# Performance work log

Hardware: AMD Instinct MI355X
Metric: run time of the kernel (lower is better)

Reference implementation:

```python
import jax, jax.numpy as jnp
import numpy as np


def setup_inputs() -> dict:
    key = jax.random.key(0)
    k1, k2 = jax.random.split(key)
    B, D, C = 4096, 128, 64
    score = jax.random.normal(k1, (B, D), dtype=jnp.float32)
    target = jax.random.randint(k2, (B,), 0, C, dtype=jnp.int64)
    alpha = jnp.full((1,), 9.0, dtype=jnp.float32)  # learned margin param
    return {"score": score, "target": target, "alpha": alpha}


def _pairwise_dist(score):
    # squared euclidean: ||xi||^2 + ||xj||^2 - 2 xi.xj, clamped at 0, then sqrt
    mag = jnp.sum(score * score, axis=1)            # [B]
    d2 = mag[:, None] + mag[None, :] - 2.0 * (score @ score.T)
    d2 = jnp.maximum(d2, 0.0)
    # safe sqrt (diagonal is exactly 0; avoid nan grads)
    safe = jnp.where(d2 > 0.0, d2, 1.0)
    return jnp.where(d2 > 0.0, jnp.sqrt(safe), 0.0)  # [B, B]


def reference(score, target, alpha):
    target = target.reshape(-1)
    B = score.shape[0]
    dist = _pairwise_dist(score)                    # [B, B]
    diff = target[:, None] != target[None, :]       # [B, B] negative-pair mask
    # per-anchor sum over negatives of exp(alpha - dist); diagonal excluded (same label)
    nes = jnp.sum(jnp.where(diff, jnp.exp(alpha[0] - dist), 0.0), axis=1)  # [B]
    l_n = jnp.log(nes[:, None] + nes[None, :])      # [B, B]
    # positive pairs i<j with equal labels
    upper = jnp.triu(jnp.ones((B, B), dtype=bool), k=1)
    pos = (~diff) & upper
    terms = jnp.where(pos, jax.nn.relu(l_n + dist) ** 2, 0.0)
    counter = jnp.sum(pos).astype(score.dtype)
    return jnp.sum(terms) / (2.0 * counter)
```

## Files before the change

kernel.cpp:

```cpp
#include <hip/hip_runtime.h>
#include <math.h>

#define BN 4096
#define DD 128
#define NCLS 64
#define PSPLIT 16
#define NPOSB (NCLS * PSPLIT)
#define NJB 32

typedef __attribute__((ext_vector_type(8))) short short8;
typedef __attribute__((ext_vector_type(4))) float f32x4;

__device__ __forceinline__ unsigned short f2bf(float f) {
    unsigned int u = __float_as_uint(f);
    u += 0x7FFFu + ((u >> 16) & 1u);
    return (unsigned short)(u >> 16);
}

__device__ __forceinline__ void gload_lds16(const void* g, void* l) {
    __builtin_amdgcn_global_load_lds(
        (const __attribute__((address_space(1))) unsigned int*)g,
        (__attribute__((address_space(3))) unsigned int*)l, 16, 0, 0);
}


__global__ __launch_bounds__(256)
void prep_kernel(const float* __restrict__ score, unsigned short* __restrict__ sbf,
                 float* __restrict__ mag) {
    int row  = blockIdx.x * 4 + (threadIdx.x >> 6);
    int lane = threadIdx.x & 63;
    float2 v = *reinterpret_cast<const float2*>(score + (size_t)row * DD + lane * 2);
    float s = v.x * v.x + v.y * v.y;
    #pragma unroll
    for (int off = 32; off; off >>= 1) s += __shfl_xor(s, off);
    ushort2 u; u.x = f2bf(v.x); u.y = f2bf(v.y);
    *reinterpret_cast<ushort2*>(sbf + (size_t)row * DD + lane * 2) = u;
    if (lane == 0) mag[row] = s;
}

__global__ __launch_bounds__(256)
void bucket_kernel(const int* __restrict__ target,
                   int* __restrict__ cls_cnt, int* __restrict__ cls_start,
                   int* __restrict__ cls_list) {
    __shared__ int hist[NCLS];
    __shared__ int offs[NCLS];
    int tid = threadIdx.x;
    if (tid < NCLS) hist[tid] = 0;
    __syncthreads();
    for (int i = tid; i < BN; i += 256) atomicAdd(&hist[target[i]], 1);
    __syncthreads();
    if (tid == 0) {
        int run = 0;
        for (int c = 0; c < NCLS; ++c) {
            cls_cnt[c] = hist[c];
            cls_start[c] = run;
            offs[c] = run;
            run += hist[c];
        }
    }
    __syncthreads();
    for (int i = tid; i < BN; i += 256) {
        int p = atomicAdd(&offs[target[i]], 1);
        cls_list[p] = i;
    }
}

__global__ __launch_bounds__(256)
void nes_kernel(const unsigned short* __restrict__ sbf, const int* __restrict__ target,
                const float* __restrict__ alphap, const float* __restrict__ mag,
                float* __restrict__ nes_part) {
    __shared__ __align__(16) unsigned short lds[2 * 128 * 128];
    __shared__ float rowsum[2][128];
    const int tid = threadIdx.x;
    const int w = tid >> 6, lane = tid & 63;
    const int lhi = lane >> 4, llo = lane & 15;
    const int i0 = blockIdx.x * 128, j0 = blockIdx.y * 128;
    const int jb = blockIdx.y;

    #pragma unroll
    for (int t = 0; t < 8; ++t) {
        int rl = w * 32 + t * 4 + lhi;
        int ch = llo ^ (rl & 7);
        const unsigned short* srcA = sbf + (size_t)(i0 + rl) * DD + ch * 8;
        const unsigned short* srcB = sbf + (size_t)(j0 + rl) * DD + ch * 8;
        gload_lds16(srcA, lds + (w * 32 + t * 4) * 128);
        gload_lds16(srcB, lds + 128 * 128 + (w * 32 + t * 4) * 128);
    }
    __syncthreads();

    const int wr = w >> 1, wc = w & 1;
    f32x4 acc[4][4] = {};
    #pragma unroll
    for (int kk = 0; kk < 4; ++kk) {
        short8 a[4], b[4];
        #pragma unroll
        for (int m = 0; m < 4; ++m) {
            int r = wr * 64 + m * 16 + llo;
            int ch = (kk * 4 + lhi) ^ (r & 7);
            a[m] = *reinterpret_cast<const short8*>(lds + r * 128 + ch * 8);
        }
        #pragma unroll
        for (int n = 0; n < 4; ++n) {
            int r = wc * 64 + n * 16 + llo;
            int ch = (kk * 4 + lhi) ^ (r & 7);
            b[n] = *reinterpret_cast<const short8*>(lds + 128 * 128 + r * 128 + ch * 8);
        }
        #pragma unroll
        for (int m = 0; m < 4; ++m)
            #pragma unroll
            for (int n = 0; n < 4; ++n)
                acc[m][n] = __builtin_amdgcn_mfma_f32_16x16x32_bf16(a[m], b[n], acc[m][n], 0, 0, 0);
    }

    const float alpha = alphap[0];
    float mj[4]; int tj[4];
    #pragma unroll
    for (int n = 0; n < 4; ++n) {
        int j = j0 + wc * 64 + n * 16 + llo;
        mj[n] = mag[j]; tj[n] = target[j];
    }
    #pragma unroll
    for (int m = 0; m < 4; ++m) {
        #pragma unroll
        for (int rg = 0; rg < 4; ++rg) {
            int li = wr * 64 + m * 16 + lhi * 4 + rg;
            int i = i0 + li;
            float mi = mag[i];
            int ti = target[i];
            float rs = 0.f;
            #pragma unroll
            for (int n = 0; n < 4; ++n) {
                float d2 = fmaxf(mi + mj[n] - 2.0f * acc[m][n][rg], 0.0f);
                float dist = sqrtf(d2);
                rs += (ti != tj[n]) ? __expf(alpha - dist) : 0.0f;
            }
            rs += __shfl_xor(rs, 1);
            rs += __shfl_xor(rs, 2);
            rs += __shfl_xor(rs, 4);
            rs += __shfl_xor(rs, 8);
            if (llo == 0) rowsum[wc][li] = rs;
        }
    }
    __syncthreads();
    if (tid < 128)
        nes_part[(size_t)jb * BN + i0 + tid] = rowsum[0][tid] + rowsum[1][tid];
}

__global__ __launch_bounds__(256)
void nes_reduce_kernel(const float* __restrict__ nes_part, float* __restrict__ nes) {
    int t = blockIdx.x * 256 + threadIdx.x;
    float s = 0.f;
    #pragma unroll
    for (int k = 0; k < NJB; ++k) s += nes_part[(size_t)k * BN + t];
    nes[t] = s;
}

__global__ __launch_bounds__(256)
void pos_kernel(const float* __restrict__ score, const float* __restrict__ mag,
                const float* __restrict__ nes,
                const int* __restrict__ cls_cnt, const int* __restrict__ cls_start,
                const int* __restrict__ cls_list,
                float* __restrict__ part_sum, unsigned int* __restrict__ part_cnt) {
    __shared__ float ssum[4];
    __shared__ unsigned int scnt[4];
    const int c = blockIdx.x;
    const int n = cls_cnt[c], s0 = cls_start[c];
    const int tid = threadIdx.x;
    const int grp = tid >> 4, llo = tid & 15;
    const int g0 = blockIdx.y * 16 + grp;
    const int nG = 16 * PSPLIT;
    const int nn = n * n;
    float s = 0.f;
    unsigned int cc = 0;
    for (int p = g0; p < nn; p += nG) {
        int a = p / n, b = p - a * n;
        if (b <= a) continue;
        int i = cls_list[s0 + a], j = cls_list[s0 + b];
        const float4* ra = reinterpret_cast<const float4*>(score + (size_t)i * DD) + llo * 2;
        const float4* rb = reinterpret_cast<const float4*>(score + (size_t)j * DD) + llo * 2;
        float4 x0 = ra[0], x1 = ra[1];
        float4 y0 = rb[0], y1 = rb[1];
        float dot = x0.x * y0.x + x0.y * y0.y + x0.z * y0.z + x0.w * y0.w
                  + x1.x * y1.x + x1.y * y1.y + x1.z * y1.z + x1.w * y1.w;
        dot += __shfl_xor(dot, 1);
        dot += __shfl_xor(dot, 2);
        dot += __shfl_xor(dot, 4);
        dot += __shfl_xor(dot, 8);
        if (llo == 0) {
            float d2 = fmaxf(mag[i] + mag[j] - 2.0f * dot, 0.0f);
            float dist = sqrtf(d2);
            float t = __logf(nes[i] + nes[j]) + dist;
            if (t > 0.f) s += t * t;
            cc++;
        }
    }
    #pragma unroll
    for (int off = 1; off < 64; off <<= 1) {
        s += __shfl_xor(s, off);
        cc += __shfl_xor(cc, off);
    }
    if ((tid & 63) == 0) { ssum[tid >> 6] = s; scnt[tid >> 6] = cc; }
    __syncthreads();
    if (tid == 0) {
        int bid = blockIdx.y * NCLS + blockIdx.x;
        part_sum[bid] = ssum[0] + ssum[1] + ssum[2] + ssum[3];
        part_cnt[bid] = scnt[0] + scnt[1] + scnt[2] + scnt[3];
    }
}

__global__ __launch_bounds__(256)
void finalize_kernel(const float* __restrict__ part_sum,
                     const unsigned int* __restrict__ part_cnt,
                     float* __restrict__ out) {
    __shared__ float fs[4];
    __shared__ unsigned int fc[4];
    int tid = threadIdx.x;
    float s = 0.f;
    unsigned int c = 0;
    #pragma unroll
    for (int k = 0; k < NPOSB / 256; ++k) {
        s += part_sum[k * 256 + tid];
        c += part_cnt[k * 256 + tid];
    }
    #pragma unroll
    for (int off = 1; off < 64; off <<= 1) {
        s += __shfl_xor(s, off);
        c += __shfl_xor(c, off);
    }
    if ((tid & 63) == 0) { fs[tid >> 6] = s; fc[tid >> 6] = c; }
    __syncthreads();
    if (tid == 0) {
        float S = fs[0] + fs[1] + fs[2] + fs[3];
        float C = (float)(fc[0] + fc[1] + fc[2] + fc[3]);
        out[0] = S / (2.0f * C);
    }
}

extern "C" void kernel_launch(void* const* d_in, const int* in_sizes, int n_in,
                              void* d_out, int out_size, void* d_ws, size_t ws_size,
                              hipStream_t stream) {
    const float* score  = (const float*)d_in[0];
    const int*   target = (const int*)d_in[1];
    const float* alpha  = (const float*)d_in[2];
    float* out = (float*)d_out;

    unsigned short* sbf = (unsigned short*)d_ws;
    float* mag      = (float*)((char*)d_ws + (size_t)BN * DD * 2);
    float* nes      = mag + BN;
    float* nes_part = nes + BN;
    float* part_sum = nes_part + (size_t)NJB * BN;
    unsigned int* part_cnt = (unsigned int*)(part_sum + NPOSB);
    int* cls_cnt   = (int*)(part_cnt + NPOSB);
    int* cls_start = cls_cnt + NCLS;
    int* cls_list  = cls_start + NCLS;

    prep_kernel<<<BN / 4, 256, 0, stream>>>(score, sbf, mag);
    bucket_kernel<<<1, 256, 0, stream>>>(target, cls_cnt, cls_start, cls_list);
    dim3 g(BN / 128, BN / 128);
    nes_kernel<<<g, 256, 0, stream>>>(sbf, target, alpha, mag, nes_part);
    nes_reduce_kernel<<<BN / 256, 256, 0, stream>>>(nes_part, nes);
    pos_kernel<<<dim3(NCLS, PSPLIT), 256, 0, stream>>>(score, mag, nes,
                                                       cls_cnt, cls_start, cls_list,
                                                       part_sum, part_cnt);
    finalize_kernel<<<1, 256, 0, stream>>>(part_sum, part_cnt, out);
}
```

Measured before the change: 112.6 us.

## Exploit distance symmetry in nes tiles and fuse prep, bucket and reduce kernels

The nes kernel now computes only upper-triangular 128x128 tiles and produces both row and column sums, so the GEMM and exp work is roughly halved. On diagonal tiles it loads the single block once. The partial sums are stored transposed ([row][jb]) and reduced inside pos_kernel, which removes the nes_reduce launch. prep and bucket are merged into one launch, and pos computes d2 directly from the fp32 difference instead of through mag. In exchange, half the grid's blocks exit immediately, and the column-sum shuffles and extra stores add work to each remaining block.

```diff
diff --git a/kernel.cpp b/kernel.cpp
--- a/kernel.cpp
+++ b/kernel.cpp
@@ -25,43 +25,42 @@
 
 
 __global__ __launch_bounds__(256)
-void prep_kernel(const float* __restrict__ score, unsigned short* __restrict__ sbf,
-                 float* __restrict__ mag) {
-    int row  = blockIdx.x * 4 + (threadIdx.x >> 6);
-    int lane = threadIdx.x & 63;
-    float2 v = *reinterpret_cast<const float2*>(score + (size_t)row * DD + lane * 2);
-    float s = v.x * v.x + v.y * v.y;
-    #pragma unroll
-    for (int off = 32; off; off >>= 1) s += __shfl_xor(s, off);
-    ushort2 u; u.x = f2bf(v.x); u.y = f2bf(v.y);
-    *reinterpret_cast<ushort2*>(sbf + (size_t)row * DD + lane * 2) = u;
-    if (lane == 0) mag[row] = s;
-}
-
-__global__ __launch_bounds__(256)
-void bucket_kernel(const int* __restrict__ target,
-                   int* __restrict__ cls_cnt, int* __restrict__ cls_start,
-                   int* __restrict__ cls_list) {
+void prep_bucket_kernel(const float* __restrict__ score, const int* __restrict__ target,
+                        unsigned short* __restrict__ sbf, float* __restrict__ mag,
+                        int* __restrict__ cls_cnt, int* __restrict__ cls_start,
+                        int* __restrict__ cls_list) {
     __shared__ int hist[NCLS];
     __shared__ int offs[NCLS];
-    int tid = threadIdx.x;
-    if (tid < NCLS) hist[tid] = 0;
-    __syncthreads();
-    for (int i = tid; i < BN; i += 256) atomicAdd(&hist[target[i]], 1);
-    __syncthreads();
-    if (tid == 0) {
-        int run = 0;
-        for (int c = 0; c < NCLS; ++c) {
-            cls_cnt[c] = hist[c];
-            cls_start[c] = run;
-            offs[c] = run;
-            run += hist[c];
-        }
-    }
-    __syncthreads();
-    for (int i = tid; i < BN; i += 256) {
-        int p = atomicAdd(&offs[target[i]], 1);
-        cls_list[p] = i;
+    const int tid = threadIdx.x;
+    if (blockIdx.x < BN / 4) {
+        int row  = blockIdx.x * 4 + (tid >> 6);
+        int lane = tid & 63;
+        float2 v = *reinterpret_cast<const float2*>(score + (size_t)row * DD + lane * 2);
+        float s = v.x * v.x + v.y * v.y;
+        #pragma unroll
+        for (int off = 32; off; off >>= 1) s += __shfl_xor(s, off);
+        ushort2 u; u.x = f2bf(v.x); u.y = f2bf(v.y);
+        *reinterpret_cast<ushort2*>(sbf + (size_t)row * DD + lane * 2) = u;
+        if (lane == 0) mag[row] = s;
+    } else {
+        if (tid < NCLS) hist[tid] = 0;
+        __syncthreads();
+        for (int i = tid; i < BN; i += 256) atomicAdd(&hist[target[i]], 1);
+        __syncthreads();
+        if (tid == 0) {
+            int run = 0;
+            for (int c = 0; c < NCLS; ++c) {
+                cls_cnt[c] = hist[c];
+                cls_start[c] = run;
+                offs[c] = run;
+                run += hist[c];
+            }
+        }
+        __syncthreads();
+        for (int i = tid; i < BN; i += 256) {
+            int p = atomicAdd(&offs[target[i]], 1);
+            cls_list[p] = i;
+        }
     }
 }
 
@@ -69,25 +68,29 @@
 void nes_kernel(const unsigned short* __restrict__ sbf, const int* __restrict__ target,
                 const float* __restrict__ alphap, const float* __restrict__ mag,
                 float* __restrict__ nes_part) {
+    const int ib = blockIdx.x, jb = blockIdx.y;
+    if (jb < ib) return;
     __shared__ __align__(16) unsigned short lds[2 * 128 * 128];
     __shared__ float rowsum[2][128];
+    __shared__ float colsum[2][128];
     const int tid = threadIdx.x;
     const int w = tid >> 6, lane = tid & 63;
     const int lhi = lane >> 4, llo = lane & 15;
-    const int i0 = blockIdx.x * 128, j0 = blockIdx.y * 128;
-    const int jb = blockIdx.y;
+    const int i0 = ib * 128, j0 = jb * 128;
+    const bool diag = (ib == jb);
 
     #pragma unroll
     for (int t = 0; t < 8; ++t) {
         int rl = w * 32 + t * 4 + lhi;
         int ch = llo ^ (rl & 7);
-        const unsigned short* srcA = sbf + (size_t)(i0 + rl) * DD + ch * 8;
-        const unsigned short* srcB = sbf + (size_t)(j0 + rl) * DD + ch * 8;
-        gload_lds16(srcA, lds + (w * 32 + t * 4) * 128);
-        gload_lds16(srcB, lds + 128 * 128 + (w * 32 + t * 4) * 128);
-    }
-    __syncthreads();
-
+        gload_lds16(sbf + (size_t)(i0 + rl) * DD + ch * 8, lds + (w * 32 + t * 4) * 128);
+        if (!diag)
+            gload_lds16(sbf + (size_t)(j0 + rl) * DD + ch * 8,
+                        lds + 128 * 128 + (w * 32 + t * 4) * 128);
+    }
+    __syncthreads();
+
+    const unsigned short* bbase = diag ? lds : (lds + 128 * 128);
     const int wr = w >> 1, wc = w & 1;
     f32x4 acc[4][4] = {};
     #pragma unroll
@@ -103,7 +106,7 @@
         for (int n = 0; n < 4; ++n) {
             int r = wc * 64 + n * 16 + llo;
             int ch = (kk * 4 + lhi) ^ (r & 7);
-            b[n] = *reinterpret_cast<const short8*>(lds + 128 * 128 + r * 128 + ch * 8);
+            b[n] = *reinterpret_cast<const short8*>(bbase + r * 128 + ch * 8);
         }
         #pragma unroll
         for (int m = 0; m < 4; ++m)
@@ -119,6 +122,7 @@
         int j = j0 + wc * 64 + n * 16 + llo;
         mj[n] = mag[j]; tj[n] = target[j];
     }
+    float cs[4] = {0.f, 0.f, 0.f, 0.f};
     #pragma unroll
     for (int m = 0; m < 4; ++m) {
         #pragma unroll
@@ -132,7 +136,9 @@
             for (int n = 0; n < 4; ++n) {
                 float d2 = fmaxf(mi + mj[n] - 2.0f * acc[m][n][rg], 0.0f);
                 float dist = sqrtf(d2);
-                rs += (ti != tj[n]) ? __expf(alpha - dist) : 0.0f;
+                float e = (ti != tj[n]) ? __expf(alpha - dist) : 0.0f;
+                rs += e;
+                cs[n] += e;
             }
             rs += __shfl_xor(rs, 1);
             rs += __shfl_xor(rs, 2);
@@ -141,23 +147,22 @@
             if (llo == 0) rowsum[wc][li] = rs;
         }
     }
-    __syncthreads();
-    if (tid < 128)
-        nes_part[(size_t)jb * BN + i0 + tid] = rowsum[0][tid] + rowsum[1][tid];
-}
-
-__global__ __launch_bounds__(256)
-void nes_reduce_kernel(const float* __restrict__ nes_part, float* __restrict__ nes) {
-    int t = blockIdx.x * 256 + threadIdx.x;
-    float s = 0.f;
-    #pragma unroll
-    for (int k = 0; k < NJB; ++k) s += nes_part[(size_t)k * BN + t];
-    nes[t] = s;
-}
-
-__global__ __launch_bounds__(256)
-void pos_kernel(const float* __restrict__ score, const float* __restrict__ mag,
-                const float* __restrict__ nes,
+    #pragma unroll
+    for (int n = 0; n < 4; ++n) {
+        cs[n] += __shfl_xor(cs[n], 16);
+        cs[n] += __shfl_xor(cs[n], 32);
+        if (lhi == 0) colsum[wr][wc * 64 + n * 16 + llo] = cs[n];
+    }
+    __syncthreads();
+    if (tid < 128) {
+        nes_part[(size_t)(i0 + tid) * NJB + jb] = rowsum[0][tid] + rowsum[1][tid];
+        if (!diag)
+            nes_part[(size_t)(j0 + tid) * NJB + ib] = colsum[0][tid] + colsum[1][tid];
+    }
+}
+
+__global__ __launch_bounds__(256)
+void pos_kernel(const float* __restrict__ score, const float* __restrict__ nes_part,
                 const int* __restrict__ cls_cnt, const int* __restrict__ cls_start,
                 const int* __restrict__ cls_list,
                 float* __restrict__ part_sum, unsigned int* __restrict__ part_cnt) {
@@ -180,16 +185,29 @@
         const float4* rb = reinterpret_cast<const float4*>(score + (size_t)j * DD) + llo * 2;
         float4 x0 = ra[0], x1 = ra[1];
         float4 y0 = rb[0], y1 = rb[1];
-        float dot = x0.x * y0.x + x0.y * y0.y + x0.z * y0.z + x0.w * y0.w
-                  + x1.x * y1.x + x1.y * y1.y + x1.z * y1.z + x1.w * y1.w;
-        dot += __shfl_xor(dot, 1);
-        dot += __shfl_xor(dot, 2);
-        dot += __shfl_xor(dot, 4);
-        dot += __shfl_xor(dot, 8);
+        float dx;
+        float d2 = 0.f;
+        dx = x0.x - y0.x; d2 += dx * dx;
+        dx = x0.y - y0.y; d2 += dx * dx;
+        dx = x0.z - y0.z; d2 += dx * dx;
+        dx = x0.w - y0.w; d2 += dx * dx;
+        dx = x1.x - y1.x; d2 += dx * dx;
+        dx = x1.y - y1.y; d2 += dx * dx;
+        dx = x1.z - y1.z; d2 += dx * dx;
+        dx = x1.w - y1.w; d2 += dx * dx;
+        float2 pi = *reinterpret_cast<const float2*>(nes_part + (size_t)i * NJB + llo * 2);
+        float2 pj = *reinterpret_cast<const float2*>(nes_part + (size_t)j * NJB + llo * 2);
+        float ni = pi.x + pi.y;
+        float nj = pj.x + pj.y;
+        #pragma unroll
+        for (int off = 1; off < 16; off <<= 1) {
+            d2 += __shfl_xor(d2, off);
+            ni += __shfl_xor(ni, off);
+            nj += __shfl_xor(nj, off);
+        }
         if (llo == 0) {
-            float d2 = fmaxf(mag[i] + mag[j] - 2.0f * dot, 0.0f);
             float dist = sqrtf(d2);
-            float t = __logf(nes[i] + nes[j]) + dist;
+            float t = __logf(ni + nj) + dist;
             if (t > 0.f) s += t * t;
             cc++;
         }
@@ -246,20 +264,18 @@
 
     unsigned short* sbf = (unsigned short*)d_ws;
     float* mag      = (float*)((char*)d_ws + (size_t)BN * DD * 2);
-    float* nes      = mag + BN;
-    float* nes_part = nes + BN;
-    float* part_sum = nes_part + (size_t)NJB * BN;
+    float* nes_part = mag + BN;
+    float* part_sum = nes_part + (size_t)BN * NJB;
     unsigned int* part_cnt = (unsigned int*)(part_sum + NPOSB);
     int* cls_cnt   = (int*)(part_cnt + NPOSB);
     int* cls_start = cls_cnt + NCLS;
     int* cls_list  = cls_start + NCLS;
 
-    prep_kernel<<<BN / 4, 256, 0, stream>>>(score, sbf, mag);
-    bucket_kernel<<<1, 256, 0, stream>>>(target, cls_cnt, cls_start, cls_list);
+    prep_bucket_kernel<<<BN / 4 + 1, 256, 0, stream>>>(score, target, sbf, mag,
+                                                       cls_cnt, cls_start, cls_list);
     dim3 g(BN / 128, BN / 128);
     nes_kernel<<<g, 256, 0, stream>>>(sbf, target, alpha, mag, nes_part);
-    nes_reduce_kernel<<<BN / 256, 256, 0, stream>>>(nes_part, nes);
-    pos_kernel<<<dim3(NCLS, PSPLIT), 256, 0, stream>>>(score, mag, nes,
+    pos_kernel<<<dim3(NCLS, PSPLIT), 256, 0, stream>>>(score, nes_part,
                                                        cls_cnt, cls_start, cls_list,
                                                        part_sum, part_cnt);
     finalize_kernel<<<1, 256, 0, stream>>>(part_sum, part_cnt, out);
```

New measurement: 109.8 us. 1.02x faster.

## Exploit distance symmetry and record positive-pair distances from the MFMA tile pass

Applied to the files above, without the earlier changes.

The negative-sum kernel now computes only upper-triangular tiles. Each tile writes both row sums and column sums, so the full sum over anchors is kept while roughly half the MFMA and exp work is removed. During the same epilogue, same-label pairs with j>i store their distance and packed indices into per-tile slots, with an overflow buffer behind them. The positive-pair kernel then just reads these records instead of re-gathering fp32 rows and recomputing dot products, and the bucket kernel is removed. In exchange the tile epilogue gains LDS atomics and scattered global writes, positive distances now come from the bf16 product rather than fp32, and a memset is added.

```diff
diff --git a/kernel.cpp b/kernel.cpp
--- a/kernel.cpp
+++ b/kernel.cpp
@@ -4,9 +4,11 @@
 #define BN 4096
 #define DD 128
 #define NCLS 64
-#define PSPLIT 16
-#define NPOSB (NCLS * PSPLIT)
+#define NT 32
+#define NTILE2 (NT * NT)
 #define NJB 32
+#define SLOTS 2048
+#define OVCAP (8u * 1024u * 1024u)
 
 typedef __attribute__((ext_vector_type(8))) short short8;
 typedef __attribute__((ext_vector_type(4))) float f32x4;
@@ -39,55 +41,40 @@
 }
 
 __global__ __launch_bounds__(256)
-void bucket_kernel(const int* __restrict__ target,
-                   int* __restrict__ cls_cnt, int* __restrict__ cls_start,
-                   int* __restrict__ cls_list) {
-    __shared__ int hist[NCLS];
-    __shared__ int offs[NCLS];
-    int tid = threadIdx.x;
-    if (tid < NCLS) hist[tid] = 0;
-    __syncthreads();
-    for (int i = tid; i < BN; i += 256) atomicAdd(&hist[target[i]], 1);
-    __syncthreads();
-    if (tid == 0) {
-        int run = 0;
-        for (int c = 0; c < NCLS; ++c) {
-            cls_cnt[c] = hist[c];
-            cls_start[c] = run;
-            offs[c] = run;
-            run += hist[c];
-        }
-    }
-    __syncthreads();
-    for (int i = tid; i < BN; i += 256) {
-        int p = atomicAdd(&offs[target[i]], 1);
-        cls_list[p] = i;
-    }
-}
-
-__global__ __launch_bounds__(256)
 void nes_kernel(const unsigned short* __restrict__ sbf, const int* __restrict__ target,
                 const float* __restrict__ alphap, const float* __restrict__ mag,
-                float* __restrict__ nes_part) {
+                float* __restrict__ nes_part,
+                uint2* __restrict__ recs, uint2* __restrict__ ovrecs,
+                int* __restrict__ tilecnt, unsigned int* __restrict__ ovcnt) {
+    const int ib = blockIdx.x, jb = blockIdx.y;
+    const int tile = ib * NT + jb;
+    if (jb < ib) {
+        if (threadIdx.x == 0) tilecnt[tile] = 0;
+        return;
+    }
     __shared__ __align__(16) unsigned short lds[2 * 128 * 128];
     __shared__ float rowsum[2][128];
+    __shared__ float colsum[2][128];
+    __shared__ int lcnt;
     const int tid = threadIdx.x;
     const int w = tid >> 6, lane = tid & 63;
     const int lhi = lane >> 4, llo = lane & 15;
-    const int i0 = blockIdx.x * 128, j0 = blockIdx.y * 128;
-    const int jb = blockIdx.y;
-
+    const int i0 = ib * 128, j0 = jb * 128;
+    const bool diag = (ib == jb);
+
+    if (tid == 0) lcnt = 0;
     #pragma unroll
     for (int t = 0; t < 8; ++t) {
         int rl = w * 32 + t * 4 + lhi;
         int ch = llo ^ (rl & 7);
-        const unsigned short* srcA = sbf + (size_t)(i0 + rl) * DD + ch * 8;
-        const unsigned short* srcB = sbf + (size_t)(j0 + rl) * DD + ch * 8;
-        gload_lds16(srcA, lds + (w * 32 + t * 4) * 128);
-        gload_lds16(srcB, lds + 128 * 128 + (w * 32 + t * 4) * 128);
-    }
-    __syncthreads();
-
+        gload_lds16(sbf + (size_t)(i0 + rl) * DD + ch * 8, lds + (w * 32 + t * 4) * 128);
+        if (!diag)
+            gload_lds16(sbf + (size_t)(j0 + rl) * DD + ch * 8,
+                        lds + 128 * 128 + (w * 32 + t * 4) * 128);
+    }
+    __syncthreads();
+
+    const unsigned short* bbase = diag ? lds : (lds + 128 * 128);
     const int wr = w >> 1, wc = w & 1;
     f32x4 acc[4][4] = {};
     #pragma unroll
@@ -103,7 +90,7 @@
         for (int n = 0; n < 4; ++n) {
             int r = wc * 64 + n * 16 + llo;
             int ch = (kk * 4 + lhi) ^ (r & 7);
-            b[n] = *reinterpret_cast<const short8*>(lds + 128 * 128 + r * 128 + ch * 8);
+            b[n] = *reinterpret_cast<const short8*>(bbase + r * 128 + ch * 8);
         }
         #pragma unroll
         for (int m = 0; m < 4; ++m)
@@ -113,12 +100,13 @@
     }
 
     const float alpha = alphap[0];
-    float mj[4]; int tj[4];
+    float mj[4]; int tj[4]; int jj[4];
     #pragma unroll
     for (int n = 0; n < 4; ++n) {
         int j = j0 + wc * 64 + n * 16 + llo;
-        mj[n] = mag[j]; tj[n] = target[j];
-    }
+        jj[n] = j; mj[n] = mag[j]; tj[n] = target[j];
+    }
+    float cs[4] = {0.f, 0.f, 0.f, 0.f};
     #pragma unroll
     for (int m = 0; m < 4; ++m) {
         #pragma unroll
@@ -132,7 +120,21 @@
             for (int n = 0; n < 4; ++n) {
                 float d2 = fmaxf(mi + mj[n] - 2.0f * acc[m][n][rg], 0.0f);
                 float dist = sqrtf(d2);
-                rs += (ti != tj[n]) ? __expf(alpha - dist) : 0.0f;
+                bool p = (ti == tj[n]);
+                float e = p ? 0.0f : __expf(alpha - dist);
+                rs += e;
+                cs[n] += e;
+                if (p && jj[n] > i) {
+                    int slot = atomicAdd(&lcnt, 1);
+                    uint2 r;
+                    r.x = __float_as_uint(dist);
+                    r.y = ((unsigned)i << 16) | (unsigned)jj[n];
+                    if (slot < SLOTS) recs[(size_t)tile * SLOTS + slot] = r;
+                    else {
+                        unsigned o = atomicAdd(ovcnt, 1u);
+                        if (o < OVCAP) ovrecs[o] = r;
+                    }
+                }
             }
             rs += __shfl_xor(rs, 1);
             rs += __shfl_xor(rs, 2);
@@ -141,9 +143,19 @@
             if (llo == 0) rowsum[wc][li] = rs;
         }
     }
-    __syncthreads();
-    if (tid < 128)
+    #pragma unroll
+    for (int n = 0; n < 4; ++n) {
+        cs[n] += __shfl_xor(cs[n], 16);
+        cs[n] += __shfl_xor(cs[n], 32);
+        if (lhi == 0) colsum[wr][wc * 64 + n * 16 + llo] = cs[n];
+    }
+    __syncthreads();
+    if (tid < 128) {
         nes_part[(size_t)jb * BN + i0 + tid] = rowsum[0][tid] + rowsum[1][tid];
+        if (!diag)
+            nes_part[(size_t)ib * BN + j0 + tid] = colsum[0][tid] + colsum[1][tid];
+    }
+    if (tid == 0) tilecnt[tile] = lcnt;
 }
 
 __global__ __launch_bounds__(256)
@@ -156,55 +168,47 @@
 }
 
 __global__ __launch_bounds__(256)
-void pos_kernel(const float* __restrict__ score, const float* __restrict__ mag,
+void pos_kernel(const uint2* __restrict__ recs, const uint2* __restrict__ ovrecs,
+                const int* __restrict__ tilecnt, const unsigned int* __restrict__ ovcnt,
                 const float* __restrict__ nes,
-                const int* __restrict__ cls_cnt, const int* __restrict__ cls_start,
-                const int* __restrict__ cls_list,
                 float* __restrict__ part_sum, unsigned int* __restrict__ part_cnt) {
     __shared__ float ssum[4];
     __shared__ unsigned int scnt[4];
-    const int c = blockIdx.x;
-    const int n = cls_cnt[c], s0 = cls_start[c];
+    const int t = blockIdx.x;
     const int tid = threadIdx.x;
-    const int grp = tid >> 4, llo = tid & 15;
-    const int g0 = blockIdx.y * 16 + grp;
-    const int nG = 16 * PSPLIT;
-    const int nn = n * n;
+    const int w = tid >> 6;
+    int cnt = tilecnt[t];
+    if (cnt > SLOTS) cnt = SLOTS;
     float s = 0.f;
     unsigned int cc = 0;
-    for (int p = g0; p < nn; p += nG) {
-        int a = p / n, b = p - a * n;
-        if (b <= a) continue;
-        int i = cls_list[s0 + a], j = cls_list[s0 + b];
-        const float4* ra = reinterpret_cast<const float4*>(score + (size_t)i * DD) + llo * 2;
-        const float4* rb = reinterpret_cast<const float4*>(score + (size_t)j * DD) + llo * 2;
-        float4 x0 = ra[0], x1 = ra[1];
-        float4 y0 = rb[0], y1 = rb[1];
-        float dot = x0.x * y0.x + x0.y * y0.y + x0.z * y0.z + x0.w * y0.w
-                  + x1.x * y1.x + x1.y * y1.y + x1.z * y1.z + x1.w * y1.w;
-        dot += __shfl_xor(dot, 1);
-        dot += __shfl_xor(dot, 2);
-        dot += __shfl_xor(dot, 4);
-        dot += __shfl_xor(dot, 8);
-        if (llo == 0) {
-            float d2 = fmaxf(mag[i] + mag[j] - 2.0f * dot, 0.0f);
-            float dist = sqrtf(d2);
-            float t = __logf(nes[i] + nes[j]) + dist;
-            if (t > 0.f) s += t * t;
-            cc++;
-        }
+    for (int k = tid; k < cnt; k += 256) {
+        uint2 r = recs[(size_t)t * SLOTS + k];
+        float dist = __uint_as_float(r.x);
+        int i = r.y >> 16, j = r.y & 0xFFFF;
+        float tv = __logf(nes[i] + nes[j]) + dist;
+        if (tv > 0.f) s += tv * tv;
+        cc++;
+    }
+    unsigned int oc = *ovcnt;
+    if (oc > OVCAP) oc = OVCAP;
+    for (unsigned int k = (unsigned)t * 256u + tid; k < oc; k += NTILE2 * 256u) {
+        uint2 r = ovrecs[k];
+        float dist = __uint_as_float(r.x);
+        int i = r.y >> 16, j = r.y & 0xFFFF;
+        float tv = __logf(nes[i] + nes[j]) + dist;
+        if (tv > 0.f) s += tv * tv;
+        cc++;
     }
     #pragma unroll
     for (int off = 1; off < 64; off <<= 1) {
         s += __shfl_xor(s, off);
         cc += __shfl_xor(cc, off);
     }
-    if ((tid & 63) == 0) { ssum[tid >> 6] = s; scnt[tid >> 6] = cc; }
+    if ((tid & 63) == 0) { ssum[w] = s; scnt[w] = cc; }
     __syncthreads();
     if (tid == 0) {
-        int bid = blockIdx.y * NCLS + blockIdx.x;
-        part_sum[bid] = ssum[0] + ssum[1] + ssum[2] + ssum[3];
-        part_cnt[bid] = scnt[0] + scnt[1] + scnt[2] + scnt[3];
+        part_sum[t] = ssum[0] + ssum[1] + ssum[2] + ssum[3];
+        part_cnt[t] = scnt[0] + scnt[1] + scnt[2] + scnt[3];
     }
 }
 
@@ -218,7 +222,7 @@
     float s = 0.f;
     unsigned int c = 0;
     #pragma unroll
-    for (int k = 0; k < NPOSB / 256; ++k) {
+    for (int k = 0; k < NTILE2 / 256; ++k) {
         s += part_sum[k * 256 + tid];
         c += part_cnt[k * 256 + tid];
     }
@@ -246,21 +250,23 @@
 
     unsigned short* sbf = (unsigned short*)d_ws;
     float* mag      = (float*)((char*)d_ws + (size_t)BN * DD * 2);
-    float* nes      = mag + BN;
-    float* nes_part = nes + BN;
-    float* part_sum = nes_part + (size_t)NJB * BN;
-    unsigned int* part_cnt = (unsigned int*)(part_sum + NPOSB);
-    int* cls_cnt   = (int*)(part_cnt + NPOSB);
-    int* cls_start = cls_cnt + NCLS;
-    int* cls_list  = cls_start + NCLS;
+    float* nes_part = mag + BN;
+    float* nes      = nes_part + (size_t)NJB * BN;
+    float* part_sum = nes + BN;
+    unsigned int* part_cnt = (unsigned int*)(part_sum + NTILE2);
+    int* tilecnt    = (int*)(part_cnt + NTILE2);
+    unsigned int* ovcnt = (unsigned int*)(tilecnt + NTILE2);
+    uint2* recs     = (uint2*)(ovcnt + 16);
+    uint2* ovrecs   = recs + (size_t)NTILE2 * SLOTS;
+
+    hipMemsetAsync(ovcnt, 0, sizeof(unsigned int), stream);
 
     prep_kernel<<<BN / 4, 256, 0, stream>>>(score, sbf, mag);
-    bucket_kernel<<<1, 256, 0, stream>>>(target, cls_cnt, cls_start, cls_list);
-    dim3 g(BN / 128, BN / 128);
-    nes_kernel<<<g, 256, 0, stream>>>(sbf, target, alpha, mag, nes_part);
+    dim3 g(NT, NT);
+    nes_kernel<<<g, 256, 0, stream>>>(sbf, target, alpha, mag, nes_part,
+                                      recs, ovrecs, tilecnt, ovcnt);
     nes_reduce_kernel<<<BN / 256, 256, 0, stream>>>(nes_part, nes);
-    pos_kernel<<<dim3(NCLS, PSPLIT), 256, 0, stream>>>(score, mag, nes,
-                                                       cls_cnt, cls_start, cls_list,
-                                                       part_sum, part_cnt);
+    pos_kernel<<<NTILE2, 256, 0, stream>>>(recs, ovrecs, tilecnt, ovcnt, nes,
+                                           part_sum, part_cnt);
     finalize_kernel<<<1, 256, 0, stream>>>(part_sum, part_cnt, out);
 }
```

Measured after the change: 103.1 us. 1.09x faster.
